# Kernel optimization log

Measured on AMD Instinct MI355X. Metric: run time of the kernel, lower is better.

## Reference

```python
import jax, jax.numpy as jnp
import numpy as np

NEG_INF = -1e15  # matches masked_fill value -1000000000000000.0
ALPHA = 0.2      # leakyReLU negative slope


def setup_inputs() -> dict:
    key = jax.random.key(0)
    k1, k2, k3, k4 = jax.random.split(key, 4)
    N, F_IN, F_OUT = 8192, 256, 64
    x = jax.random.normal(k1, (N, F_IN), dtype=jnp.float32)
    mask = jax.random.randint(k2, (N, N), 0, 2, dtype=jnp.int32)
    trans = jax.random.normal(k3, (F_IN, F_OUT), dtype=jnp.float32) * 0.1
    attn = jax.random.normal(k4, (2 * F_OUT, 1), dtype=jnp.float32) * 0.1
    return {"x": x, "mask": mask, "trans": trans, "attn": attn}


def reference(x, mask, trans, attn):
    d = trans.shape[1]
    h = x @ trans                                  # [N, d]
    e1 = h @ attn[:d, :]                           # [N, 1]
    e2 = h @ attn[d:, :]                           # [N, 1]
    scores = jax.nn.leaky_relu(e1 + e2.T, negative_slope=ALPHA)  # [N, N]
    masked = jnp.where(mask == 0, NEG_INF, scores)
    attention = jax.nn.softmax(masked, axis=1)
    return attention @ h                           # [N, d]
```

## Files before the change

### kernel.cpp

```cpp
#include <hip/hip_runtime.h>
#include <hip/hip_bf16.h>
#include <math.h>

#define N 8192
#define FIN 256
#define D 64
#define ALPHA 0.2f
#define CS 2048

typedef __attribute__((ext_vector_type(8))) short bf16x8;
typedef __attribute__((ext_vector_type(4))) float f32x4;
typedef __attribute__((ext_vector_type(4))) int i32x4;

__global__ __launch_bounds__(256) void k_h_e(
    const float* __restrict__ x, const float* __restrict__ trans,
    const float* __restrict__ attn,
    __hip_bfloat16* __restrict__ hF, float* __restrict__ e1, float* __restrict__ e2)
{
    __shared__ float xs[8 * FIN];
    __shared__ __hip_bfloat16 hl[8 * D];
    const int t = threadIdx.x;
    const int r0 = blockIdx.x * 8;

    #pragma unroll
    for (int v = 0; v < 2; ++v) {
        int idx = t + 256 * v;
        ((float4*)xs)[idx] = ((const float4*)(x + (size_t)r0 * FIN))[idx];
    }
    __syncthreads();

    const int lane = t & 63, w = t >> 6;
    const float* xa = xs + (2 * w) * FIN;
    const float* xb = xs + (2 * w + 1) * FIN;
    float acca = 0.f, accb = 0.f;
    #pragma unroll 8
    for (int k = 0; k < FIN; ++k) {
        const float tv = trans[k * D + lane];
        acca = fmaf(xa[k], tv, acca);
        accb = fmaf(xb[k], tv, accb);
    }
    const int ra = r0 + 2 * w, rb = ra + 1;

    const float a1 = attn[lane], a2 = attn[D + lane];
    float p1a = acca * a1, p2a = acca * a2;
    float p1b = accb * a1, p2b = accb * a2;
    #pragma unroll
    for (int mm = 1; mm <= 32; mm <<= 1) {
        p1a += __shfl_xor(p1a, mm);
        p2a += __shfl_xor(p2a, mm);
        p1b += __shfl_xor(p1b, mm);
        p2b += __shfl_xor(p2b, mm);
    }
    if (lane == 0) { e1[ra] = p1a; e2[ra] = p2a; e1[rb] = p1b; e2[rb] = p2b; }

    hl[(2 * w) * D + lane]     = __float2bfloat16(acca);
    hl[(2 * w + 1) * D + lane] = __float2bfloat16(accb);
    __syncthreads();
    if (t < D) {
        const int q = t >> 4, m = t & 15;
        const int cb = r0 >> 5, jgrp = (r0 >> 3) & 3;
        union { bf16x8 v; __hip_bfloat16 h[8]; } o;
        #pragma unroll
        for (int r = 0; r < 8; ++r) o.h[r] = hl[r * D + q * 16 + m];
        *(bf16x8*)(hF + (((size_t)cb * 4 + q) * 64 + jgrp * 16 + m) * 8) = o.v;
    }
}

__global__ __launch_bounds__(256, 3) void k_attn(
    const int* __restrict__ mask, const __hip_bfloat16* __restrict__ hF,
    const float* __restrict__ e1, const float* __restrict__ e2,
    float* __restrict__ out)
{
    __shared__ float cw[4 * 16 * 64];
    __shared__ float lw[4][16];
    const int t = threadIdx.x;
    const int lane = t & 63, wave = t >> 6;
    const int i0 = blockIdx.x * 16;
    const int c0 = wave * CS;
    const int m = lane & 15, quad = lane >> 4;
    const int row = i0 + m;
    const float er = e1[row];

    const __hip_bfloat16* hfp = hF + (((size_t)(c0 >> 5)) * 4 * 64 + lane) * 8;
    const i32x4* mp = (const i32x4*)(mask + (size_t)row * N + c0 + quad * 8);
    const float* ep = e2 + c0 + quad * 8;

    f32x4 acc0 = {0.f, 0.f, 0.f, 0.f};
    f32x4 acc1 = {0.f, 0.f, 0.f, 0.f};
    f32x4 acc2 = {0.f, 0.f, 0.f, 0.f};
    f32x4 acc3 = {0.f, 0.f, 0.f, 0.f};
    float lsum = 0.f;

    i32x4 pmA0 = __builtin_nontemporal_load(mp + 0);
    i32x4 pmB0 = __builtin_nontemporal_load(mp + 1);
    i32x4 pmA1 = __builtin_nontemporal_load(mp + 8);
    i32x4 pmB1 = __builtin_nontemporal_load(mp + 9);
    i32x4 pmA2 = __builtin_nontemporal_load(mp + 16);
    i32x4 pmB2 = __builtin_nontemporal_load(mp + 17);
    i32x4 pmA3 = __builtin_nontemporal_load(mp + 24);
    i32x4 pmB3 = __builtin_nontemporal_load(mp + 25);

    bf16x8 pb0 = *(const bf16x8*)(hfp);
    bf16x8 pb1 = *(const bf16x8*)(hfp + 512);
    bf16x8 pb2 = *(const bf16x8*)(hfp + 1024);
    bf16x8 pb3 = *(const bf16x8*)(hfp + 1536);
    float4 pea = *(const float4*)(ep);
    float4 peb = *(const float4*)(ep + 4);

#define ITER(J, IT, LASTC4)                                                    \
    {                                                                          \
        const i32x4 m0 = pmA##J, m1 = pmB##J;                                  \
        if (!(LASTC4)) {                                                       \
            pmA##J = __builtin_nontemporal_load(mp + ((IT) + 4) * 8);          \
            pmB##J = __builtin_nontemporal_load(mp + ((IT) + 4) * 8 + 1);      \
        }                                                                      \
        const bf16x8 b0 = pb0, b1 = pb1, b2 = pb2, b3 = pb3;                   \
        const float4 ea = pea, eb = peb;                                       \
        if ((IT) < 63) {                                                       \
            const size_t ito = (size_t)((IT) + 1) * 2048;                      \
            pb0 = *(const bf16x8*)(hfp + ito);                                 \
            pb1 = *(const bf16x8*)(hfp + ito + 512);                           \
            pb2 = *(const bf16x8*)(hfp + ito + 1024);                          \
            pb3 = *(const bf16x8*)(hfp + ito + 1536);                          \
            pea = *(const float4*)(ep + ((IT) + 1) * 32);                      \
            peb = *(const float4*)(ep + ((IT) + 1) * 32 + 4);                  \
        }                                                                      \
        float s0 = er + ea.x; s0 = s0 > 0.f ? s0 : ALPHA * s0;                 \
        float s1 = er + ea.y; s1 = s1 > 0.f ? s1 : ALPHA * s1;                 \
        float s2 = er + ea.z; s2 = s2 > 0.f ? s2 : ALPHA * s2;                 \
        float s3 = er + ea.w; s3 = s3 > 0.f ? s3 : ALPHA * s3;                 \
        float s4 = er + eb.x; s4 = s4 > 0.f ? s4 : ALPHA * s4;                 \
        float s5 = er + eb.y; s5 = s5 > 0.f ? s5 : ALPHA * s5;                 \
        float s6 = er + eb.z; s6 = s6 > 0.f ? s6 : ALPHA * s6;                 \
        float s7 = er + eb.w; s7 = s7 > 0.f ? s7 : ALPHA * s7;                 \
        const float p0 = m0[0] ? __expf(s0) : 0.f;                             \
        const float p1 = m0[1] ? __expf(s1) : 0.f;                             \
        const float p2 = m0[2] ? __expf(s2) : 0.f;                             \
        const float p3 = m0[3] ? __expf(s3) : 0.f;                             \
        const float p4 = m1[0] ? __expf(s4) : 0.f;                             \
        const float p5 = m1[1] ? __expf(s5) : 0.f;                             \
        const float p6 = m1[2] ? __expf(s6) : 0.f;                             \
        const float p7 = m1[3] ? __expf(s7) : 0.f;                             \
        union { bf16x8 v; __hip_bfloat162 h2[4]; } af;                         \
        af.h2[0] = __float22bfloat162_rn(make_float2(p0, p1));                 \
        af.h2[1] = __float22bfloat162_rn(make_float2(p2, p3));                 \
        af.h2[2] = __float22bfloat162_rn(make_float2(p4, p5));                 \
        af.h2[3] = __float22bfloat162_rn(make_float2(p6, p7));                 \
        lsum += ((p0 + p1) + (p2 + p3)) + ((p4 + p5) + (p6 + p7));             \
        acc0 = __builtin_amdgcn_mfma_f32_16x16x32_bf16(af.v, b0, acc0, 0, 0, 0); \
        acc1 = __builtin_amdgcn_mfma_f32_16x16x32_bf16(af.v, b1, acc1, 0, 0, 0); \
        acc2 = __builtin_amdgcn_mfma_f32_16x16x32_bf16(af.v, b2, acc2, 0, 0, 0); \
        acc3 = __builtin_amdgcn_mfma_f32_16x16x32_bf16(af.v, b3, acc3, 0, 0, 0); \
    }

    for (int c4 = 0; c4 < 16; ++c4) {
        const int base = c4 * 4;
        const bool lastc4 = (c4 == 15);
        ITER(0, base + 0, lastc4)
        ITER(1, base + 1, lastc4)
        ITER(2, base + 2, lastc4)
        ITER(3, base + 3, lastc4)
    }
#undef ITER

    lsum += __shfl_xor(lsum, 16);
    lsum += __shfl_xor(lsum, 32);
    if (quad == 0) lw[wave][m] = lsum;

    #pragma unroll
    for (int reg = 0; reg < 4; ++reg) {
        float* rbase = cw + (wave * 16 + quad * 4 + reg) * 64;
        rbase[m     ] = acc0[reg];
        rbase[m + 16] = acc1[reg];
        rbase[m + 32] = acc2[reg];
        rbase[m + 48] = acc3[reg];
    }
    __syncthreads();
    #pragma unroll
    for (int rr = 0; rr < 4; ++rr) {
        const int idx = rr * 256 + t;
        const int r = idx >> 6, c = idx & 63;
        float s = ((cw[(0 * 16 + r) * 64 + c] + cw[(1 * 16 + r) * 64 + c])
                +   cw[(2 * 16 + r) * 64 + c]) + cw[(3 * 16 + r) * 64 + c];
        float l = ((lw[0][r] + lw[1][r]) + lw[2][r]) + lw[3][r];
        out[(size_t)(i0 + r) * D + c] = s / l;
    }
}

extern "C" void kernel_launch(void* const* d_in, const int* in_sizes, int n_in,
                              void* d_out, int out_size, void* d_ws, size_t ws_size,
                              hipStream_t stream) {
    const float* x     = (const float*)d_in[0];
    const int*   mask  = (const int*)d_in[1];
    const float* trans = (const float*)d_in[2];
    const float* attn  = (const float*)d_in[3];
    float* out = (float*)d_out;

    char* ws = (char*)d_ws;
    __hip_bfloat16* hF = (__hip_bfloat16*)ws;
    char* p = ws + (size_t)D * N * sizeof(__hip_bfloat16);
    float* e1 = (float*)p;            p += (size_t)N * sizeof(float);
    float* e2 = (float*)p;            p += (size_t)N * sizeof(float);

    k_h_e<<<N / 8, 256, 0, stream>>>(x, trans, attn, hF, e1, e2);
    k_attn<<<N / 16, 256, 0, stream>>>(mask, hF, e1, e2, out);
}
```

Baseline: 402.1 us.

## Stage mask tiles into LDS via async global_load_lds double buffering

Replaces the per-lane nontemporal register prefetch of the int32 mask with direct global-to-LDS DMA loads (global_load_lds), double-buffered per wave, with explicit vmcnt waits between halves. The aim is to issue fully coalesced mask loads and free the registers that held the prefetched mask, improving overlap of the dominant mask stream with the exp and MFMA work. In exchange it uses 64KB of LDS per block and drops the occupancy hint in launch bounds. It also relies on hand-coded waitcnt values, which are fragile if the compiler reorders or adds memory ops.

```diff
diff --git a/kernel.cpp b/kernel.cpp
--- a/kernel.cpp
+++ b/kernel.cpp
@@ -7,10 +7,10 @@
 #define D 64
 #define ALPHA 0.2f
 #define CS 2048
+#define HBYTES 8192
 
 typedef __attribute__((ext_vector_type(8))) short bf16x8;
 typedef __attribute__((ext_vector_type(4))) float f32x4;
-typedef __attribute__((ext_vector_type(4))) int i32x4;
 
 __global__ __launch_bounds__(256) void k_h_e(
     const float* __restrict__ x, const float* __restrict__ trans,
@@ -66,23 +66,36 @@
     }
 }
 
-__global__ __launch_bounds__(256, 3) void k_attn(
+__device__ __forceinline__ void stage_half(const char* gs, char* ld) {
+    #pragma unroll
+    for (int i = 0; i < 8; ++i) {
+        __builtin_amdgcn_global_load_lds(
+            (const __attribute__((address_space(1))) void*)(gs + (size_t)i * (2u * N * 4u)),
+            (__attribute__((address_space(3))) void*)(ld + i * 1024),
+            16, 0, 2 );
+    }
+}
+
+__global__ __launch_bounds__(256) void k_attn(
     const int* __restrict__ mask, const __hip_bfloat16* __restrict__ hF,
     const float* __restrict__ e1, const float* __restrict__ e2,
     float* __restrict__ out)
 {
-    __shared__ float cw[4 * 16 * 64];
+    __shared__ __align__(16) char smem[4 * 2 * HBYTES];
     __shared__ float lw[4][16];
     const int t = threadIdx.x;
     const int lane = t & 63, wave = t >> 6;
     const int i0 = blockIdx.x * 16;
     const int c0 = wave * CS;
     const int m = lane & 15, quad = lane >> 4;
-    const int row = i0 + m;
-    const float er = e1[row];
+    const float er = e1[i0 + m];
+
+    char* sw = smem + wave * (2 * HBYTES);
+    const char* gdma = (const char*)(mask + (size_t)(i0 + (lane >> 5)) * N
+                                          + c0 + (lane & 31) * 4);
+    const int moff = m * 512 + quad * 32;
 
     const __hip_bfloat16* hfp = hF + (((size_t)(c0 >> 5)) * 4 * 64 + lane) * 8;
-    const i32x4* mp = (const i32x4*)(mask + (size_t)row * N + c0 + quad * 8);
     const float* ep = e2 + c0 + quad * 8;
 
     f32x4 acc0 = {0.f, 0.f, 0.f, 0.f};
@@ -91,14 +104,8 @@
     f32x4 acc3 = {0.f, 0.f, 0.f, 0.f};
     float lsum = 0.f;
 
-    i32x4 pmA0 = __builtin_nontemporal_load(mp + 0);
-    i32x4 pmB0 = __builtin_nontemporal_load(mp + 1);
-    i32x4 pmA1 = __builtin_nontemporal_load(mp + 8);
-    i32x4 pmB1 = __builtin_nontemporal_load(mp + 9);
-    i32x4 pmA2 = __builtin_nontemporal_load(mp + 16);
-    i32x4 pmB2 = __builtin_nontemporal_load(mp + 17);
-    i32x4 pmA3 = __builtin_nontemporal_load(mp + 24);
-    i32x4 pmB3 = __builtin_nontemporal_load(mp + 25);
+    stage_half(gdma,        sw + lane * 16);
+    stage_half(gdma + 512,  sw + HBYTES + lane * 16);
 
     bf16x8 pb0 = *(const bf16x8*)(hfp);
     bf16x8 pb1 = *(const bf16x8*)(hfp + 512);
@@ -107,23 +114,20 @@
     float4 pea = *(const float4*)(ep);
     float4 peb = *(const float4*)(ep + 4);
 
-#define ITER(J, IT, LASTC4)                                                    \
+#define ITER(P, ITN, PREF)                                                     \
     {                                                                          \
-        const i32x4 m0 = pmA##J, m1 = pmB##J;                                  \
-        if (!(LASTC4)) {                                                       \
-            pmA##J = __builtin_nontemporal_load(mp + ((IT) + 4) * 8);          \
-            pmB##J = __builtin_nontemporal_load(mp + ((IT) + 4) * 8 + 1);      \
-        }                                                                      \
+        const int4 mm0 = *(const int4*)(sb + moff + (P) * 128);                \
+        const int4 mm1 = *(const int4*)(sb + moff + (P) * 128 + 16);           \
         const bf16x8 b0 = pb0, b1 = pb1, b2 = pb2, b3 = pb3;                   \
         const float4 ea = pea, eb = peb;                                       \
-        if ((IT) < 63) {                                                       \
-            const size_t ito = (size_t)((IT) + 1) * 2048;                      \
+        if (PREF) {                                                            \
+            const size_t ito = (size_t)((ITN) + 1) * 2048;                     \
             pb0 = *(const bf16x8*)(hfp + ito);                                 \
             pb1 = *(const bf16x8*)(hfp + ito + 512);                           \
             pb2 = *(const bf16x8*)(hfp + ito + 1024);                          \
             pb3 = *(const bf16x8*)(hfp + ito + 1536);                          \
-            pea = *(const float4*)(ep + ((IT) + 1) * 32);                      \
-            peb = *(const float4*)(ep + ((IT) + 1) * 32 + 4);                  \
+            pea = *(const float4*)(ep + ((ITN) + 1) * 32);                     \
+            peb = *(const float4*)(ep + ((ITN) + 1) * 32 + 4);                 \
         }                                                                      \
         float s0 = er + ea.x; s0 = s0 > 0.f ? s0 : ALPHA * s0;                 \
         float s1 = er + ea.y; s1 = s1 > 0.f ? s1 : ALPHA * s1;                 \
@@ -133,14 +137,14 @@
         float s5 = er + eb.y; s5 = s5 > 0.f ? s5 : ALPHA * s5;                 \
         float s6 = er + eb.z; s6 = s6 > 0.f ? s6 : ALPHA * s6;                 \
         float s7 = er + eb.w; s7 = s7 > 0.f ? s7 : ALPHA * s7;                 \
-        const float p0 = m0[0] ? __expf(s0) : 0.f;                             \
-        const float p1 = m0[1] ? __expf(s1) : 0.f;                             \
-        const float p2 = m0[2] ? __expf(s2) : 0.f;                             \
-        const float p3 = m0[3] ? __expf(s3) : 0.f;                             \
-        const float p4 = m1[0] ? __expf(s4) : 0.f;                             \
-        const float p5 = m1[1] ? __expf(s5) : 0.f;                             \
-        const float p6 = m1[2] ? __expf(s6) : 0.f;                             \
-        const float p7 = m1[3] ? __expf(s7) : 0.f;                             \
+        const float p0 = mm0.x ? __expf(s0) : 0.f;                             \
+        const float p1 = mm0.y ? __expf(s1) : 0.f;                             \
+        const float p2 = mm0.z ? __expf(s2) : 0.f;                             \
+        const float p3 = mm0.w ? __expf(s3) : 0.f;                             \
+        const float p4 = mm1.x ? __expf(s4) : 0.f;                             \
+        const float p5 = mm1.y ? __expf(s5) : 0.f;                             \
+        const float p6 = mm1.z ? __expf(s6) : 0.f;                             \
+        const float p7 = mm1.w ? __expf(s7) : 0.f;                             \
         union { bf16x8 v; __hip_bfloat162 h2[4]; } af;                         \
         af.h2[0] = __float22bfloat162_rn(make_float2(p0, p1));                 \
         af.h2[1] = __float22bfloat162_rn(make_float2(p2, p3));                 \
@@ -153,13 +157,27 @@
         acc3 = __builtin_amdgcn_mfma_f32_16x16x32_bf16(af.v, b3, acc3, 0, 0, 0); \
     }
 
-    for (int c4 = 0; c4 < 16; ++c4) {
-        const int base = c4 * 4;
-        const bool lastc4 = (c4 == 15);
-        ITER(0, base + 0, lastc4)
-        ITER(1, base + 1, lastc4)
-        ITER(2, base + 2, lastc4)
-        ITER(3, base + 3, lastc4)
+    for (int h = 0; h < 15; ++h) {
+        __builtin_amdgcn_s_waitcnt(0x0F7E);
+        __builtin_amdgcn_sched_barrier(0);
+        const char* sb = sw + (h & 1) * HBYTES;
+        const int itb = h * 4;
+        ITER(0, itb + 0, true)
+        ITER(1, itb + 1, true)
+        ITER(2, itb + 2, true)
+        ITER(3, itb + 3, true)
+        if (h < 14)
+            stage_half(gdma + (size_t)(h + 2) * 512,
+                       sw + (h & 1) * HBYTES + lane * 16);
+    }
+    {
+        __builtin_amdgcn_s_waitcnt(0x0F76);
+        __builtin_amdgcn_sched_barrier(0);
+        const char* sb = sw + HBYTES;
+        ITER(0, 60, true)
+        ITER(1, 61, true)
+        ITER(2, 62, true)
+        ITER(3, 63, false)
     }
 #undef ITER
 
@@ -167,6 +185,8 @@
     lsum += __shfl_xor(lsum, 32);
     if (quad == 0) lw[wave][m] = lsum;
 
+    __syncthreads();
+    float* cw = (float*)smem;
     #pragma unroll
     for (int reg = 0; reg < 4; ++reg) {
         float* rbase = cw + (wave * 16 + quad * 4 + reg) * 64;
```

New measurement: 377.3 us. 6.2% less time.
